# Kernel optimization log

Measured on AMD Instinct MI355X. Metric: run time of the kernel, lower is better.

Reference implementation:

```python
import jax, jax.numpy as jnp
import numpy as np

NUM_TOKENS = 16384
MODEL_DIM = 4096
MAX_EXPERTS = 128
INITIAL_EXPERTS = 64
THRESHOLD = 0.5  # rm_threshold


def setup_inputs() -> dict:
    key = jax.random.key(0)
    k1, k2 = jax.random.split(key)
    x = jax.random.normal(k1, (NUM_TOKENS, MODEL_DIM), dtype=jnp.float32)
    # Linear(model_dim, max_expert_num, bias=False).weight -> [E_max, D]
    wg_weight = jax.random.normal(k2, (MAX_EXPERTS, MODEL_DIM), dtype=jnp.float32) * (1.0 / np.sqrt(MODEL_DIM))
    # experts_mask: first `INITIAL_EXPERTS` active
    experts_mask = (jnp.arange(MAX_EXPERTS) < INITIAL_EXPERTS).astype(jnp.float32)
    return {"x": x, "wg_weight": wg_weight, "experts_mask": experts_mask}


def reference(x, wg_weight, experts_mask):
    # gate logits: [N, E_max]
    scores = jnp.einsum("nd,ed->ne", x, wg_weight)
    # mask inactive experts
    scores = jnp.where(experts_mask[None, :] == 0, jnp.float32(-1e9), scores)
    # fp32 softmax + epsilon (matches F.softmax(..., dtype=float32) + 1e-14)
    scores = jax.nn.softmax(scores.astype(jnp.float32), axis=-1) + 1e-14
    # sort descending along expert dim
    sorted_scores = -jnp.sort(-scores, axis=-1)
    cum_scores = jnp.cumsum(sorted_scores, axis=-1)
    # adaptive top-k: experts needed to accumulate THRESHOLD routing mass
    mask = (cum_scores - sorted_scores) < THRESHOLD
    top_k = mask.sum(axis=-1).astype(jnp.int32)
    active_experts = experts_mask.sum().astype(jnp.int32)
    top_k = jnp.minimum(top_k, active_experts)
    return scores.astype(x.dtype), top_k
```

## Files before the change

kernel.cpp:

```cpp
#include <hip/hip_runtime.h>
#include <hip/hip_bf16.h>
#include <stdint.h>

#define NTOK 16384
#define DDIM 4096
#define NEXP 128
#define BM 32
#define BK 64
#define NT (DDIM / BK)

typedef __attribute__((ext_vector_type(8))) short short8;
typedef __attribute__((ext_vector_type(4))) float f32x4;
typedef __attribute__((address_space(1))) const uint32_t gu32;
typedef __attribute__((address_space(3))) uint32_t lu32;

__device__ __forceinline__ void gload16(const void* g, void* l) {
    __builtin_amdgcn_global_load_lds((gu32*)g, (lu32*)l, 16, 0, 0);
}

__device__ __forceinline__ void split_bf16(float f, uint32_t& h, uint32_t& l) {
    uint32_t u = __float_as_uint(f);
    h = (u + 0x7FFFu + ((u >> 16) & 1u)) >> 16;
    float r = f - __uint_as_float(h << 16);
    uint32_t v = __float_as_uint(r);
    l = (v + 0x7FFFu + ((v >> 16) & 1u)) >> 16;
}

__global__ void prep_w(const float* __restrict__ w,
                       uint16_t* __restrict__ whi, uint16_t* __restrict__ wlo) {
    int i = (blockIdx.x * blockDim.x + threadIdx.x) * 4;
    float4 f = *(const float4*)(w + i);
    uint32_t h0, h1, h2, h3, l0, l1, l2, l3;
    split_bf16(f.x, h0, l0);
    split_bf16(f.y, h1, l1);
    split_bf16(f.z, h2, l2);
    split_bf16(f.w, h3, l3);
    uint2 hv = make_uint2(h0 | (h1 << 16), h2 | (h3 << 16));
    uint2 lv = make_uint2(l0 | (l1 << 16), l2 | (l3 << 16));
    *(uint2*)(whi + i) = hv;
    *(uint2*)(wlo + i) = lv;
}

__global__ __launch_bounds__(256) void gemm_logits(
    const float* __restrict__ x,
    const uint16_t* __restrict__ whi, const uint16_t* __restrict__ wlo,
    float* __restrict__ S)
{
    __shared__ uint16_t sAh[2][BM * BK], sAl[2][BM * BK];
    __shared__ uint16_t sBh[2][NEXP * BK], sBl[2][NEXP * BK];

    const int tid  = threadIdx.x;
    const int lane = tid & 63;
    const int wave = tid >> 6;
    const int q = lane >> 4;
    const int c = lane & 15;
    const int rxor = c & 7;
    const int m0 = blockIdx.x * BM;

    const int ar = tid >> 3, aj = tid & 7;
    const float* xp = x + (size_t)(m0 + ar) * DDIM + aj * 8;
    const int aoff = ar * BK + (aj ^ (ar & 7)) * 8;

    const int brow = wave * 32 + (lane >> 3);
    const int bjj  = (lane & 7) ^ ((lane >> 3) & 7);
    const size_t bsrc = (size_t)brow * DDIM + bjj * 8;
    const int bdst = (wave * 32) * BK + lane * 8;

    f32x4 acc[2][2];
    #pragma unroll
    for (int mt = 0; mt < 2; ++mt)
        #pragma unroll
        for (int nt = 0; nt < 2; ++nt)
            acc[mt][nt] = (f32x4){0.f, 0.f, 0.f, 0.f};

    auto stageB = [&](int nxt, int kn) {
        #pragma unroll
        for (int i = 0; i < 4; ++i) {
            gload16(whi + bsrc + (size_t)(i * 8) * DDIM + kn, &sBh[nxt][bdst + i * 8 * BK]);
            gload16(wlo + bsrc + (size_t)(i * 8) * DDIM + kn, &sBl[nxt][bdst + i * 8 * BK]);
        }
    };

    auto writeA = [&](int nxt, float4 fa, float4 fb) {
        uint32_t h[8], l[8];
        split_bf16(fa.x, h[0], l[0]); split_bf16(fa.y, h[1], l[1]);
        split_bf16(fa.z, h[2], l[2]); split_bf16(fa.w, h[3], l[3]);
        split_bf16(fb.x, h[4], l[4]); split_bf16(fb.y, h[5], l[5]);
        split_bf16(fb.z, h[6], l[6]); split_bf16(fb.w, h[7], l[7]);
        uint4 hv = make_uint4(h[0] | (h[1] << 16), h[2] | (h[3] << 16),
                              h[4] | (h[5] << 16), h[6] | (h[7] << 16));
        uint4 lv = make_uint4(l[0] | (l[1] << 16), l[2] | (l[3] << 16),
                              l[4] | (l[5] << 16), l[6] | (l[7] << 16));
        *(uint4*)&sAh[nxt][aoff] = hv;
        *(uint4*)&sAl[nxt][aoff] = lv;
    };

    auto compute = [&](int cur) {
        #pragma unroll
        for (int ks = 0; ks < 2; ++ks) {
            const int off = (((ks << 2) | q) ^ rxor) << 3;
            short8 ah[2], alo[2], bh[2], blo[2];
            #pragma unroll
            for (int mt = 0; mt < 2; ++mt) {
                const int ro = (mt * 16 + c) * BK + off;
                ah[mt]  = *(const short8*)&sAh[cur][ro];
                alo[mt] = *(const short8*)&sAl[cur][ro];
            }
            #pragma unroll
            for (int nt = 0; nt < 2; ++nt) {
                const int ro = (wave * 32 + nt * 16 + c) * BK + off;
                bh[nt]  = *(const short8*)&sBh[cur][ro];
                blo[nt] = *(const short8*)&sBl[cur][ro];
            }
            #pragma unroll
            for (int mt = 0; mt < 2; ++mt)
                #pragma unroll
                for (int nt = 0; nt < 2; ++nt) {
                    acc[mt][nt] = __builtin_amdgcn_mfma_f32_16x16x32_bf16(alo[mt], bh[nt],  acc[mt][nt], 0, 0, 0);
                    acc[mt][nt] = __builtin_amdgcn_mfma_f32_16x16x32_bf16(ah[mt],  blo[nt], acc[mt][nt], 0, 0, 0);
                    acc[mt][nt] = __builtin_amdgcn_mfma_f32_16x16x32_bf16(ah[mt],  bh[nt],  acc[mt][nt], 0, 0, 0);
                }
        }
    };

    {
        float4 fa = *(const float4*)(xp);
        float4 fb = *(const float4*)(xp + 4);
        asm volatile("" ::: "memory");
        stageB(0, 0);
        writeA(0, fa, fb);
        asm volatile("s_waitcnt vmcnt(0) lgkmcnt(0)" ::: "memory");
        __builtin_amdgcn_s_barrier();
    }

    #pragma unroll 2
    for (int t = 0; t < NT - 1; ++t) {
        const int cur = t & 1, nxt = cur ^ 1;
        const int kn = (t + 1) * BK;
        float4 fa = *(const float4*)(xp + kn);
        float4 fb = *(const float4*)(xp + kn + 4);
        asm volatile("" ::: "memory");
        stageB(nxt, kn);
        asm volatile("s_waitcnt vmcnt(10)" ::: "memory");
        compute(cur);
        writeA(nxt, fa, fb);
        asm volatile("s_waitcnt lgkmcnt(0)" ::: "memory");
        __builtin_amdgcn_s_barrier();
    }
    asm volatile("s_waitcnt vmcnt(0)" ::: "memory");
    compute((NT - 1) & 1);

    #pragma unroll
    for (int mt = 0; mt < 2; ++mt)
        #pragma unroll
        for (int nt = 0; nt < 2; ++nt) {
            const int e = wave * 32 + nt * 16 + c;
            #pragma unroll
            for (int r = 0; r < 4; ++r) {
                const int tok = m0 + mt * 16 + q * 4 + r;
                S[(size_t)tok * NEXP + e] = acc[mt][nt][r];
            }
        }
}

__global__ __launch_bounds__(256) void postproc(
    float* __restrict__ S, const float* __restrict__ mask,
    float* __restrict__ topk_out)
{
    const int lane = threadIdx.x & 63;
    const int wave = threadIdx.x >> 6;
    const int g  = lane >> 3;
    const int gl = lane & 7;
    const int tok = blockIdx.x * 32 + wave * 8 + g;
    float* row = S + (size_t)tok * NEXP + gl * 16;
    const float* mrow = mask + gl * 16;

    float v[16];
    #pragma unroll
    for (int i = 0; i < 4; ++i)
        *(float4*)&v[i * 4] = *(const float4*)&row[i * 4];

    bool act[16];
    int cnt = 0;
    float mx = -3.0e38f;
    #pragma unroll
    for (int j = 0; j < 16; ++j) {
        act[j] = (mrow[j] != 0.f);
        cnt += act[j] ? 1 : 0;
        mx = fmaxf(mx, act[j] ? v[j] : -3.0e38f);
    }
    int active = cnt;
    #pragma unroll
    for (int off = 4; off; off >>= 1) active += __shfl_xor(active, off);
    #pragma unroll
    for (int off = 4; off; off >>= 1) mx = fmaxf(mx, __shfl_xor(mx, off));

    float sum = 0.f;
    #pragma unroll
    for (int j = 0; j < 16; ++j) {
        v[j] = act[j] ? __expf(v[j] - mx) : 0.f;
        sum += v[j];
    }
    #pragma unroll
    for (int off = 4; off; off >>= 1) sum += __shfl_xor(sum, off);

    const float inv = 1.0f / sum;
    #pragma unroll
    for (int j = 0; j < 16; ++j) v[j] = v[j] * inv + 1e-14f;
    #pragma unroll
    for (int i = 0; i < 4; ++i)
        *(float4*)&row[i * 4] = *(const float4*)&v[i * 4];

    float cum = 0.f;
    int k = 0;
    const int base = gl * 16;
    for (int it = 0; it < 33; ++it) {
        float lm = v[0];
        int lj = 0;
        #pragma unroll
        for (int j = 1; j < 16; ++j) {
            const bool gt = v[j] > lm;
            lm = gt ? v[j] : lm;
            lj = gt ? j : lj;
        }
        unsigned long long key =
            ((unsigned long long)__float_as_uint(lm) << 32) | (unsigned)(base + lj);
        #pragma unroll
        for (int off = 4; off; off >>= 1) {
            unsigned long long o = __shfl_xor(key, off);
            key = (o > key) ? o : key;
        }
        const float mv = __uint_as_float((uint32_t)(key >> 32));
        const int widx = (int)(key & 127u);
        k += (cum < 0.5f) ? 1 : 0;
        cum += mv;
        #pragma unroll
        for (int j = 0; j < 16; ++j)
            v[j] = (widx == base + j) ? 0.f : v[j];
    }
    int topk = k < active ? k : active;
    if (gl == 0) topk_out[tok] = (float)topk;
}

extern "C" void kernel_launch(void* const* d_in, const int* in_sizes, int n_in,
                              void* d_out, int out_size, void* d_ws, size_t ws_size,
                              hipStream_t stream) {
    (void)in_sizes; (void)n_in; (void)out_size; (void)ws_size;
    const float* x    = (const float*)d_in[0];
    const float* w    = (const float*)d_in[1];
    const float* mask = (const float*)d_in[2];

    float* S    = (float*)d_out;
    float* topk = S + (size_t)NTOK * NEXP;

    uint16_t* whi = (uint16_t*)d_ws;
    uint16_t* wlo = whi + (size_t)NEXP * DDIM;

    hipLaunchKernelGGL(prep_w, dim3((NEXP * DDIM) / (256 * 4)), dim3(256), 0, stream,
                       w, whi, wlo);
    hipLaunchKernelGGL(gemm_logits, dim3(NTOK / BM), dim3(256), 0, stream,
                       x, whi, wlo, S);
    hipLaunchKernelGGL(postproc, dim3(NTOK / 32), dim3(256), 0, stream,
                       S, mask, topk);
}
```

Before: 477.3 us.

## Load weight fragments directly from global into registers, drop B LDS staging

```diff
diff --git a/kernel.cpp b/kernel.cpp
--- a/kernel.cpp
+++ b/kernel.cpp
@@ -11,12 +11,6 @@
 
 typedef __attribute__((ext_vector_type(8))) short short8;
 typedef __attribute__((ext_vector_type(4))) float f32x4;
-typedef __attribute__((address_space(1))) const uint32_t gu32;
-typedef __attribute__((address_space(3))) uint32_t lu32;
-
-__device__ __forceinline__ void gload16(const void* g, void* l) {
-    __builtin_amdgcn_global_load_lds((gu32*)g, (lu32*)l, 16, 0, 0);
-}
 
 __device__ __forceinline__ void split_bf16(float f, uint32_t& h, uint32_t& l) {
     uint32_t u = __float_as_uint(f);
@@ -41,13 +35,12 @@
     *(uint2*)(wlo + i) = lv;
 }
 
-__global__ __launch_bounds__(256) void gemm_logits(
+__global__ __launch_bounds__(256, 4) void gemm_logits(
     const float* __restrict__ x,
     const uint16_t* __restrict__ whi, const uint16_t* __restrict__ wlo,
     float* __restrict__ S)
 {
     __shared__ uint16_t sAh[2][BM * BK], sAl[2][BM * BK];
-    __shared__ uint16_t sBh[2][NEXP * BK], sBl[2][NEXP * BK];
 
     const int tid  = threadIdx.x;
     const int lane = tid & 63;
@@ -61,10 +54,9 @@
     const float* xp = x + (size_t)(m0 + ar) * DDIM + aj * 8;
     const int aoff = ar * BK + (aj ^ (ar & 7)) * 8;
 
-    const int brow = wave * 32 + (lane >> 3);
-    const int bjj  = (lane & 7) ^ ((lane >> 3) & 7);
-    const size_t bsrc = (size_t)brow * DDIM + bjj * 8;
-    const int bdst = (wave * 32) * BK + lane * 8;
+    const size_t brow = (size_t)(wave * 32 + c) * DDIM + q * 8;
+    const uint16_t* bh_p = whi + brow;
+    const uint16_t* bl_p = wlo + brow;
 
     f32x4 acc[2][2];
     #pragma unroll
@@ -72,14 +64,6 @@
         #pragma unroll
         for (int nt = 0; nt < 2; ++nt)
             acc[mt][nt] = (f32x4){0.f, 0.f, 0.f, 0.f};
-
-    auto stageB = [&](int nxt, int kn) {
-        #pragma unroll
-        for (int i = 0; i < 4; ++i) {
-            gload16(whi + bsrc + (size_t)(i * 8) * DDIM + kn, &sBh[nxt][bdst + i * 8 * BK]);
-            gload16(wlo + bsrc + (size_t)(i * 8) * DDIM + kn, &sBl[nxt][bdst + i * 8 * BK]);
-        }
-    };
 
     auto writeA = [&](int nxt, float4 fa, float4 fb) {
         uint32_t h[8], l[8];
@@ -95,11 +79,38 @@
         *(uint4*)&sAl[nxt][aoff] = lv;
     };
 
-    auto compute = [&](int cur) {
+    {
+        float4 fa = *(const float4*)(xp);
+        float4 fb = *(const float4*)(xp + 4);
+        writeA(0, fa, fb);
+        __syncthreads();
+    }
+
+    #pragma unroll 2
+    for (int t = 0; t < NT; ++t) {
+        const int cur = t & 1;
+        const int k0 = t * BK;
+
+        short8 bh[2][2], bl[2][2];
+        #pragma unroll
+        for (int nt = 0; nt < 2; ++nt)
+            #pragma unroll
+            for (int ks = 0; ks < 2; ++ks) {
+                const size_t o = (size_t)(nt * 16) * DDIM + k0 + ks * 32;
+                bh[nt][ks] = *(const short8*)(bh_p + o);
+                bl[nt][ks] = *(const short8*)(bl_p + o);
+            }
+
+        float4 fa, fb;
+        if (t + 1 < NT) {
+            fa = *(const float4*)(xp + k0 + BK);
+            fb = *(const float4*)(xp + k0 + BK + 4);
+        }
+
         #pragma unroll
         for (int ks = 0; ks < 2; ++ks) {
             const int off = (((ks << 2) | q) ^ rxor) << 3;
-            short8 ah[2], alo[2], bh[2], blo[2];
+            short8 ah[2], alo[2];
             #pragma unroll
             for (int mt = 0; mt < 2; ++mt) {
                 const int ro = (mt * 16 + c) * BK + off;
@@ -107,48 +118,20 @@
                 alo[mt] = *(const short8*)&sAl[cur][ro];
             }
             #pragma unroll
-            for (int nt = 0; nt < 2; ++nt) {
-                const int ro = (wave * 32 + nt * 16 + c) * BK + off;
-                bh[nt]  = *(const short8*)&sBh[cur][ro];
-                blo[nt] = *(const short8*)&sBl[cur][ro];
-            }
-            #pragma unroll
             for (int mt = 0; mt < 2; ++mt)
                 #pragma unroll
                 for (int nt = 0; nt < 2; ++nt) {
-                    acc[mt][nt] = __builtin_amdgcn_mfma_f32_16x16x32_bf16(alo[mt], bh[nt],  acc[mt][nt], 0, 0, 0);
-                    acc[mt][nt] = __builtin_amdgcn_mfma_f32_16x16x32_bf16(ah[mt],  blo[nt], acc[mt][nt], 0, 0, 0);
-                    acc[mt][nt] = __builtin_amdgcn_mfma_f32_16x16x32_bf16(ah[mt],  bh[nt],  acc[mt][nt], 0, 0, 0);
+                    acc[mt][nt] = __builtin_amdgcn_mfma_f32_16x16x32_bf16(alo[mt], bh[nt][ks], acc[mt][nt], 0, 0, 0);
+                    acc[mt][nt] = __builtin_amdgcn_mfma_f32_16x16x32_bf16(ah[mt],  bl[nt][ks], acc[mt][nt], 0, 0, 0);
+                    acc[mt][nt] = __builtin_amdgcn_mfma_f32_16x16x32_bf16(ah[mt],  bh[nt][ks], acc[mt][nt], 0, 0, 0);
                 }
         }
-    };
-
-    {
-        float4 fa = *(const float4*)(xp);
-        float4 fb = *(const float4*)(xp + 4);
-        asm volatile("" ::: "memory");
-        stageB(0, 0);
-        writeA(0, fa, fb);
-        asm volatile("s_waitcnt vmcnt(0) lgkmcnt(0)" ::: "memory");
-        __builtin_amdgcn_s_barrier();
-    }
-
-    #pragma unroll 2
-    for (int t = 0; t < NT - 1; ++t) {
-        const int cur = t & 1, nxt = cur ^ 1;
-        const int kn = (t + 1) * BK;
-        float4 fa = *(const float4*)(xp + kn);
-        float4 fb = *(const float4*)(xp + kn + 4);
-        asm volatile("" ::: "memory");
-        stageB(nxt, kn);
-        asm volatile("s_waitcnt vmcnt(10)" ::: "memory");
-        compute(cur);
-        writeA(nxt, fa, fb);
-        asm volatile("s_waitcnt lgkmcnt(0)" ::: "memory");
-        __builtin_amdgcn_s_barrier();
-    }
-    asm volatile("s_waitcnt vmcnt(0)" ::: "memory");
-    compute((NT - 1) & 1);
+
+        if (t + 1 < NT) {
+            writeA(cur ^ 1, fa, fb);
+            __syncthreads();
+        }
+    }
 
     #pragma unroll
     for (int mt = 0; mt < 2; ++mt)
```

Result: no change. 474.7 us (-0.5%).
